# Kernel tuning notes

Hardware: AMD Instinct MI355X
Metric: run time of the kernel (lower is better)

Reference implementation:

```python
import jax, jax.numpy as jnp
import numpy as np

B, N, NF, ND, NH = 16, 128, 64, 100, 64

def glorot(key, shape):
    fan_in, fan_out = shape[0], shape[1]
    limit = np.sqrt(6.0 / (fan_in + fan_out)).astype(np.float32)
    return jax.random.uniform(key, shape, jnp.float32, -limit, limit)

def setup_inputs() -> dict:
    key = jax.random.key(0)
    k1, k2, k3, k4, k5 = jax.random.split(key, 5)
    return {
        "atom_features": jax.random.normal(k1, (B, N, NF), jnp.float32),
        "distance_matrix": jax.random.uniform(k2, (B, N, N, ND), jnp.float32),
        "distance_matrix_mask": jnp.ones((B, N, N), jnp.float32),
        "W_cf": glorot(k3, (NF, NH)),
        "W_df": glorot(k4, (ND, NH)),
        "W_fc": glorot(k5, (NH, NF)),
        "b_cf": jnp.zeros((NH,), jnp.float32),
        "b_df": jnp.zeros((NH,), jnp.float32),
    }

def reference(atom_features, distance_matrix, distance_matrix_mask, W_cf, W_df, W_fc, b_cf, b_df):
    # dist_h: [B, N, N, H]
    dist_h = jnp.einsum('bijd,dh->bijh', distance_matrix, W_df) + b_df
    # atom_h: [B, N, H] -> broadcast over axis 1 (matches tf expand_dims axis=1)
    atom_h = jnp.einsum('bjf,fh->bjh', atom_features, W_cf) + b_cf
    gated = dist_h * atom_h[:, None, :, :]                 # [B, N, N, H]
    out = jnp.einsum('bijh,hf->bijf', gated, W_fc)          # [B, N, N, F]
    out = out * distance_matrix_mask[..., None]
    out = jnp.tanh(out)
    return jnp.sum(out, axis=2) + atom_features             # [B, N, F]
```

## Files before the change

kernel.cpp:

```cpp
#include <hip/hip_runtime.h>
#include <hip/hip_bf16.h>

#define Bsz 16
#define Nn  128
#define NFd 64
#define NDd 100
#define NHd 64

typedef __attribute__((ext_vector_type(8))) short bf16x8;
typedef __attribute__((ext_vector_type(4))) float f32x4;

__device__ __forceinline__ short f2bf(float f) {
  return (short)__builtin_bit_cast(ushort, __float2bfloat16(f));
}

__device__ __forceinline__ float fast_tanh(float x) {
  float e = __expf(2.0f * x);
  return 1.0f - 2.0f * __builtin_amdgcn_rcpf(e + 1.0f);
}

__device__ __forceinline__ void glds16(const float* g, float* l) {
  __builtin_amdgcn_global_load_lds(
      (const __attribute__((address_space(1))) void*)g,
      (__attribute__((address_space(3))) void*)l, 16, 0, 0);
}
__device__ __forceinline__ void glds4(const float* g, float* l) {
  __builtin_amdgcn_global_load_lds(
      (const __attribute__((address_space(1))) void*)g,
      (__attribute__((address_space(3))) void*)l, 4, 0, 0);
}

__global__ __launch_bounds__(256) void prep_kernel(
    const float* __restrict__ AF, const float* __restrict__ Wcf,
    const float* __restrict__ bcf, const float* __restrict__ Wdf,
    const float* __restrict__ Wfc, float* __restrict__ atomh,
    ushort* __restrict__ wdfp, ushort* __restrict__ wfcp,
    float* __restrict__ out) {
  int t = threadIdx.x;
  int blk = blockIdx.x;
  if (blk < 512) {
    int row = blk * 4 + (t >> 6);
    int h = t & 63;
    const float* af = AF + (size_t)row * NFd;
    float a0 = 0.f, a1 = 0.f, a2 = 0.f, a3 = 0.f;
    #pragma unroll 4
    for (int f = 0; f < NFd; f += 4) {
      a0 += af[f + 0] * Wcf[(f + 0) * NHd + h];
      a1 += af[f + 1] * Wcf[(f + 1) * NHd + h];
      a2 += af[f + 2] * Wcf[(f + 2) * NHd + h];
      a3 += af[f + 3] * Wcf[(f + 3) * NHd + h];
    }
    atomh[(size_t)row * NHd + h] = bcf[h] + ((a0 + a1) + (a2 + a3));
  } else if (blk < 544) {
    int idx = (blk - 512) * 256 + t;
    int e = idx & 7;
    int col = (idx >> 3) & 63;
    int grp = idx >> 9;
    int k = grp * 8 + e;
    float v = (k < NDd) ? Wdf[k * NHd + col] : 0.f;
    wdfp[idx] = (ushort)f2bf(v);
  } else if (blk < 560) {
    int idx = (blk - 544) * 256 + t;
    int e = idx & 7;
    int col = (idx >> 3) & 63;
    int grp = idx >> 9;
    int k = grp * 8 + e;
    wfcp[idx] = (ushort)f2bf(Wfc[k * NFd + col]);
  } else {
    int idx = (blk - 560) * 256 + t;
    out[idx] = AF[idx];
  }
}

__global__ __launch_bounds__(256, 6) void dtnn_main_kernel(
    const float* __restrict__ DM,
    const float* __restrict__ MASK,
    const float* __restrict__ bdf,
    const float* __restrict__ atomh,
    const ushort* __restrict__ wdfp,
    const ushort* __restrict__ wfcp,
    float* __restrict__ out) {
  __shared__ float stage[64 * 100];

  const int t    = threadIdx.x;
  const int blk  = blockIdx.x;
  const int bi   = blk >> 1;
  const int half = blk & 1;
  const int b    = bi >> 7;
  const int w    = t >> 6;
  const int lane = t & 63;
  const int p    = t & 15;
  const int q    = (t >> 4) & 3;

  const int jrow = half * 64 + w * 16;

  const float* gsrc = DM + (size_t)bi * (Nn * NDd) + (size_t)jrow * NDd;
  float* lbase = stage + w * 1600;
  #pragma unroll
  for (int v = 0; v < 6; ++v)
    glds16(gsrc + v * 256 + lane * 4, lbase + v * 256);
  glds4(gsrc + 1536 + lane, lbase + 1536);

  asm volatile("s_waitcnt vmcnt(0)" ::: "memory");
  __builtin_amdgcn_sched_barrier(0);

  const bf16x8* wdfv = reinterpret_cast<const bf16x8*>(wdfp);
  const bf16x8* wfcv = reinterpret_cast<const bf16x8*>(wfcp);

  f32x4 acc[4];
  #pragma unroll
  for (int ht = 0; ht < 4; ++ht) {
    float bv = bdf[ht * 16 + p];
    acc[ht] = (f32x4){bv, bv, bv, bv};
  }

  const float* arow = stage + (w * 16 + p) * 100;
  #pragma unroll
  for (int ks = 0; ks < 3; ++ks) {
    float4 x = *reinterpret_cast<const float4*>(arow + ks * 32 + q * 8);
    float4 y = *reinterpret_cast<const float4*>(arow + ks * 32 + q * 8 + 4);
    bf16x8 a;
    a[0] = f2bf(x.x); a[1] = f2bf(x.y); a[2] = f2bf(x.z); a[3] = f2bf(x.w);
    a[4] = f2bf(y.x); a[5] = f2bf(y.y); a[6] = f2bf(y.z); a[7] = f2bf(y.w);
    #pragma unroll
    for (int ht = 0; ht < 4; ++ht)
      acc[ht] = __builtin_amdgcn_mfma_f32_16x16x32_bf16(
          a, wdfv[(ks * 4 + q) * 64 + ht * 16 + p], acc[ht], 0, 0, 0);
  }
  {
    bf16x8 a = (bf16x8){0, 0, 0, 0, 0, 0, 0, 0};
    if (q == 0) {
      float4 x = *reinterpret_cast<const float4*>(arow + 96);
      a[0] = f2bf(x.x); a[1] = f2bf(x.y); a[2] = f2bf(x.z); a[3] = f2bf(x.w);
    }
    #pragma unroll
    for (int ht = 0; ht < 4; ++ht)
      acc[ht] = __builtin_amdgcn_mfma_f32_16x16x32_bf16(
          a, wdfv[(12 + q) * 64 + ht * 16 + p], acc[ht], 0, 0, 0);
  }

  const float* ap = atomh + ((size_t)(b * Nn + jrow + 4 * q)) * NHd + p;
  #pragma unroll
  for (int ht = 0; ht < 4; ++ht) {
    #pragma unroll
    for (int r = 0; r < 4; ++r) acc[ht][r] *= ap[r * NHd + ht * 16];
  }

  ushort* gb = reinterpret_cast<ushort*>(lbase);
  #pragma unroll
  for (int r = 0; r < 4; ++r) {
    int rr = 4 * q + r;
    int sw = (rr & 7) << 3;
    #pragma unroll
    for (int ht = 0; ht < 4; ++ht)
      gb[rr * 64 + ((ht * 16 + p) ^ sw)] = (ushort)f2bf(acc[ht][r]);
  }
  asm volatile("" ::: "memory");

  f32x4 acc2[4];
  #pragma unroll
  for (int ft = 0; ft < 4; ++ft) acc2[ft] = (f32x4){0.f, 0.f, 0.f, 0.f};

  #pragma unroll
  for (int ks = 0; ks < 2; ++ks) {
    int h0 = (ks * 32 + q * 8) ^ ((p & 7) << 3);
    bf16x8 a2 = *reinterpret_cast<const bf16x8*>(&gb[p * 64 + h0]);
    #pragma unroll
    for (int ft = 0; ft < 4; ++ft)
      acc2[ft] = __builtin_amdgcn_mfma_f32_16x16x32_bf16(
          a2, wfcv[(ks * 4 + q) * 64 + ft * 16 + p], acc2[ft], 0, 0, 0);
  }

  float s[4] = {0.f, 0.f, 0.f, 0.f};
  #pragma unroll
  for (int r = 0; r < 4; ++r) {
    float m = MASK[(size_t)bi * Nn + jrow + 4 * q + r];
    #pragma unroll
    for (int ft = 0; ft < 4; ++ft) s[ft] += fast_tanh(acc2[ft][r] * m);
  }

  #pragma unroll
  for (int ft = 0; ft < 4; ++ft) {
    s[ft] += __shfl_xor(s[ft], 16, 64);
    s[ft] += __shfl_xor(s[ft], 32, 64);
  }
  if (q == 0) {
    #pragma unroll
    for (int ft = 0; ft < 4; ++ft)
      unsafeAtomicAdd(&out[(size_t)bi * NFd + ft * 16 + p], s[ft]);
  }
}

extern "C" void kernel_launch(void* const* d_in, const int* in_sizes, int n_in,
                              void* d_out, int out_size, void* d_ws, size_t ws_size,
                              hipStream_t stream) {
  const float* AF   = (const float*)d_in[0];
  const float* DM   = (const float*)d_in[1];
  const float* MASK = (const float*)d_in[2];
  const float* Wcf  = (const float*)d_in[3];
  const float* Wdf  = (const float*)d_in[4];
  const float* Wfc  = (const float*)d_in[5];
  const float* bcf  = (const float*)d_in[6];
  const float* bdf  = (const float*)d_in[7];
  float* out = (float*)d_out;

  float*  atomh = (float*)d_ws;
  ushort* wdfp  = (ushort*)((char*)d_ws + 524288);
  ushort* wfcp  = (ushort*)((char*)d_ws + 524288 + 16384);

  prep_kernel<<<1072, 256, 0, stream>>>(AF, Wcf, bcf, Wdf, Wfc, atomh, wdfp, wfcp, out);
  dtnn_main_kernel<<<2 * Bsz * Nn, 256, 0, stream>>>(DM, MASK, bdf, atomh, wdfp, wfcp, out);
}
```

Baseline: 35.84 us.

## Stage distance tiles in swizzled column chunks and overlap loads with MFMA

Reorganizes the global-to-LDS staging of the distance-matrix tile into three 32-column chunks per row group, stored with an XOR swizzle, plus a separate tail for columns 96-99. The first GEMM then waits on partial vmcnt counts through inline asm, so each chunk's MFMAs can start while later chunks are still loading, rather than waiting for the whole tile. The swizzle is meant to cut LDS bank conflicts on the 128-bit reads. The cost is hand-written waitcnt/ds_read asm that depends on the compiler issuing the loads in a fixed order, which is fragile.

Result: slower. 38.74 us (+8.1%).

```diff
diff --git a/kernel.cpp b/kernel.cpp
--- a/kernel.cpp
+++ b/kernel.cpp
@@ -28,6 +28,20 @@
   __builtin_amdgcn_global_load_lds(
       (const __attribute__((address_space(1))) void*)g,
       (__attribute__((address_space(3))) void*)l, 4, 0, 0);
+}
+
+__device__ __forceinline__ unsigned lds_off(const void* p) {
+  return (unsigned)(uintptr_t)(const __attribute__((address_space(3))) char*)p;
+}
+
+template <int N>
+__device__ __forceinline__ void wait_read2(f32x4& x, f32x4& y, unsigned a0, unsigned a1) {
+  asm volatile("s_waitcnt vmcnt(%4)\n\t"
+               "ds_read_b128 %0, %2\n\t"
+               "ds_read_b128 %1, %3\n\t"
+               "s_waitcnt lgkmcnt(0)"
+               : "=&v"(x), "=&v"(y)
+               : "v"(a0), "v"(a1), "i"(N));
 }
 
 __global__ __launch_bounds__(256) void prep_kernel(
@@ -96,13 +110,19 @@
 
   const float* gsrc = DM + (size_t)bi * (Nn * NDd) + (size_t)jrow * NDd;
   float* lbase = stage + w * 1600;
-  #pragma unroll
-  for (int v = 0; v < 6; ++v)
-    glds16(gsrc + v * 256 + lane * 4, lbase + v * 256);
-  glds4(gsrc + 1536 + lane, lbase + 1536);
-
-  asm volatile("s_waitcnt vmcnt(0)" ::: "memory");
-  __builtin_amdgcn_sched_barrier(0);
+  {
+    const int r8 = lane >> 3, b8 = lane & 7;
+    #pragma unroll
+    for (int c = 0; c < 3; ++c) {
+      #pragma unroll
+      for (int g = 0; g < 2; ++g) {
+        int r = g * 8 + r8;
+        glds16(gsrc + r * 100 + c * 32 + ((b8 ^ (r & 7)) << 2),
+               lbase + c * 512 + g * 256);
+      }
+    }
+    glds4(gsrc + (lane >> 2) * 100 + 96 + (lane & 3), lbase + 1536);
+  }
 
   const bf16x8* wdfv = reinterpret_cast<const bf16x8*>(wdfp);
   const bf16x8* wfcv = reinterpret_cast<const bf16x8*>(wfcp);
@@ -114,24 +134,35 @@
     acc[ht] = (f32x4){bv, bv, bv, bv};
   }
 
-  const float* arow = stage + (w * 16 + p) * 100;
-  #pragma unroll
-  for (int ks = 0; ks < 3; ++ks) {
-    float4 x = *reinterpret_cast<const float4*>(arow + ks * 32 + q * 8);
-    float4 y = *reinterpret_cast<const float4*>(arow + ks * 32 + q * 8 + 4);
-    bf16x8 a;
-    a[0] = f2bf(x.x); a[1] = f2bf(x.y); a[2] = f2bf(x.z); a[3] = f2bf(x.w);
-    a[4] = f2bf(y.x); a[5] = f2bf(y.y); a[6] = f2bf(y.z); a[7] = f2bf(y.w);
-    #pragma unroll
-    for (int ht = 0; ht < 4; ++ht)
-      acc[ht] = __builtin_amdgcn_mfma_f32_16x16x32_bf16(
-          a, wdfv[(ks * 4 + q) * 64 + ht * 16 + p], acc[ht], 0, 0, 0);
-  }
+  const unsigned sbase = lds_off(lbase);
+  const unsigned arow  = sbase + p * 128;
+  const unsigned bsw0  = ((2 * q) ^ (p & 7)) << 4;
+  f32x4 x, y;
+
+  #define P1_CHUNK(KS, NW)                                                     \
+  {                                                                            \
+    unsigned a0 = arow + KS * 2048 + bsw0;                                     \
+    wait_read2<NW>(x, y, a0, a0 ^ 16);                                         \
+    bf16x8 a;                                                                  \
+    a[0] = f2bf(x[0]); a[1] = f2bf(x[1]); a[2] = f2bf(x[2]); a[3] = f2bf(x[3]);\
+    a[4] = f2bf(y[0]); a[5] = f2bf(y[1]); a[6] = f2bf(y[2]); a[7] = f2bf(y[3]);\
+    _Pragma("unroll")                                                          \
+    for (int ht = 0; ht < 4; ++ht)                                             \
+      acc[ht] = __builtin_amdgcn_mfma_f32_16x16x32_bf16(                       \
+          a, wdfv[(KS * 4 + q) * 64 + ht * 16 + p], acc[ht], 0, 0, 0);         \
+  }
+  P1_CHUNK(0, 5)
+  P1_CHUNK(1, 3)
+  P1_CHUNK(2, 1)
+  #undef P1_CHUNK
+
   {
+    asm volatile("s_waitcnt vmcnt(0)" ::: "memory");
+    __builtin_amdgcn_sched_barrier(0);
     bf16x8 a = (bf16x8){0, 0, 0, 0, 0, 0, 0, 0};
     if (q == 0) {
-      float4 x = *reinterpret_cast<const float4*>(arow + 96);
-      a[0] = f2bf(x.x); a[1] = f2bf(x.y); a[2] = f2bf(x.z); a[3] = f2bf(x.w);
+      float4 tx = *reinterpret_cast<const float4*>(lbase + 1536 + p * 4);
+      a[0] = f2bf(tx.x); a[1] = f2bf(tx.y); a[2] = f2bf(tx.z); a[3] = f2bf(tx.w);
     }
     #pragma unroll
     for (int ht = 0; ht < 4; ++ht)
```

## Swizzle DM LDS staging, transpose atom_h, prefetch gate/mask before wait

Applied to the files above, without the earlier changes.

Distance-matrix tiles are now staged into LDS in 32-column chunks with an XOR swizzle, so the MFMA A-fragment reads avoid bank conflicts. atom_h is stored transposed so each lane reads its four gating values with one vector load, and those loads plus the mask and bias loads are issued before the single vmcnt wait, overlapping with the DM transfer. The copy of atom_features into the output is folded into the atom_h prep blocks, which drops 512 prep blocks. Occupancy hint for the main kernel drops from 6 to 4 waves, which may lower latency hiding in exchange for more registers.

Result: slower. 41.65 us (+16.2%).

```diff
diff --git a/kernel.cpp b/kernel.cpp
--- a/kernel.cpp
+++ b/kernel.cpp
@@ -33,7 +33,7 @@
 __global__ __launch_bounds__(256) void prep_kernel(
     const float* __restrict__ AF, const float* __restrict__ Wcf,
     const float* __restrict__ bcf, const float* __restrict__ Wdf,
-    const float* __restrict__ Wfc, float* __restrict__ atomh,
+    const float* __restrict__ Wfc, float* __restrict__ atomhT,
     ushort* __restrict__ wdfp, ushort* __restrict__ wfcp,
     float* __restrict__ out) {
   int t = threadIdx.x;
@@ -50,7 +50,9 @@
       a2 += af[f + 2] * Wcf[(f + 2) * NHd + h];
       a3 += af[f + 3] * Wcf[(f + 3) * NHd + h];
     }
-    atomh[(size_t)row * NHd + h] = bcf[h] + ((a0 + a1) + (a2 + a3));
+    int b = row >> 7, j = row & 127;
+    atomhT[((size_t)(b * NHd + h)) << 7 | j] = bcf[h] + ((a0 + a1) + (a2 + a3));
+    out[(size_t)row * NFd + h] = af[h];
   } else if (blk < 544) {
     int idx = (blk - 512) * 256 + t;
     int e = idx & 7;
@@ -59,28 +61,25 @@
     int k = grp * 8 + e;
     float v = (k < NDd) ? Wdf[k * NHd + col] : 0.f;
     wdfp[idx] = (ushort)f2bf(v);
-  } else if (blk < 560) {
+  } else {
     int idx = (blk - 544) * 256 + t;
     int e = idx & 7;
     int col = (idx >> 3) & 63;
     int grp = idx >> 9;
     int k = grp * 8 + e;
     wfcp[idx] = (ushort)f2bf(Wfc[k * NFd + col]);
-  } else {
-    int idx = (blk - 560) * 256 + t;
-    out[idx] = AF[idx];
-  }
-}
-
-__global__ __launch_bounds__(256, 6) void dtnn_main_kernel(
+  }
+}
+
+__global__ __launch_bounds__(256, 4) void dtnn_main_kernel(
     const float* __restrict__ DM,
     const float* __restrict__ MASK,
     const float* __restrict__ bdf,
-    const float* __restrict__ atomh,
+    const float* __restrict__ atomhT,
     const ushort* __restrict__ wdfp,
     const ushort* __restrict__ wfcp,
     float* __restrict__ out) {
-  __shared__ float stage[64 * 100];
+  __shared__ float stage[4 * 1600];
 
   const int t    = threadIdx.x;
   const int blk  = blockIdx.x;
@@ -95,33 +94,49 @@
   const int jrow = half * 64 + w * 16;
 
   const float* gsrc = DM + (size_t)bi * (Nn * NDd) + (size_t)jrow * NDd;
-  float* lbase = stage + w * 1600;
-  #pragma unroll
-  for (int v = 0; v < 6; ++v)
-    glds16(gsrc + v * 256 + lane * 4, lbase + v * 256);
-  glds4(gsrc + 1536 + lane, lbase + 1536);
+  float* lb = stage + w * 1600;
+  {
+    const int r8 = lane >> 3, b8 = lane & 7;
+    #pragma unroll
+    for (int c = 0; c < 3; ++c) {
+      #pragma unroll
+      for (int g = 0; g < 2; ++g) {
+        int r = g * 8 + r8;
+        glds16(gsrc + r * 100 + c * 32 + ((b8 ^ (r & 7)) << 2),
+               lb + c * 512 + g * 256);
+      }
+    }
+    glds4(gsrc + (lane >> 2) * 100 + 96 + (lane & 3), lb + 1536);
+  }
+
+  const bf16x8* wdfv = reinterpret_cast<const bf16x8*>(wdfp);
+  const bf16x8* wfcv = reinterpret_cast<const bf16x8*>(wfcp);
+
+  f32x4 ah[4];
+  #pragma unroll
+  for (int ht = 0; ht < 4; ++ht)
+    ah[ht] = *reinterpret_cast<const f32x4*>(
+        atomhT + (((size_t)(b * NHd + ht * 16 + p)) << 7) + jrow + 4 * q);
+  f32x4 mv = *reinterpret_cast<const f32x4*>(MASK + (size_t)bi * Nn + jrow + 4 * q);
+  float bv[4];
+  #pragma unroll
+  for (int ht = 0; ht < 4; ++ht) bv[ht] = bdf[ht * 16 + p];
 
   asm volatile("s_waitcnt vmcnt(0)" ::: "memory");
   __builtin_amdgcn_sched_barrier(0);
 
-  const bf16x8* wdfv = reinterpret_cast<const bf16x8*>(wdfp);
-  const bf16x8* wfcv = reinterpret_cast<const bf16x8*>(wfcp);
-
   f32x4 acc[4];
   #pragma unroll
-  for (int ht = 0; ht < 4; ++ht) {
-    float bv = bdf[ht * 16 + p];
-    acc[ht] = (f32x4){bv, bv, bv, bv};
-  }
-
-  const float* arow = stage + (w * 16 + p) * 100;
+  for (int ht = 0; ht < 4; ++ht) acc[ht] = (f32x4){bv[ht], bv[ht], bv[ht], bv[ht]};
+
   #pragma unroll
   for (int ks = 0; ks < 3; ++ks) {
-    float4 x = *reinterpret_cast<const float4*>(arow + ks * 32 + q * 8);
-    float4 y = *reinterpret_cast<const float4*>(arow + ks * 32 + q * 8 + 4);
+    const float* cbase = lb + ks * 512 + p * 32;
+    f32x4 x = *reinterpret_cast<const f32x4*>(cbase + (((2 * q)     ) ^ (p & 7)) * 4);
+    f32x4 y = *reinterpret_cast<const f32x4*>(cbase + (((2 * q) + 1 ) ^ (p & 7)) * 4);
     bf16x8 a;
-    a[0] = f2bf(x.x); a[1] = f2bf(x.y); a[2] = f2bf(x.z); a[3] = f2bf(x.w);
-    a[4] = f2bf(y.x); a[5] = f2bf(y.y); a[6] = f2bf(y.z); a[7] = f2bf(y.w);
+    a[0] = f2bf(x[0]); a[1] = f2bf(x[1]); a[2] = f2bf(x[2]); a[3] = f2bf(x[3]);
+    a[4] = f2bf(y[0]); a[5] = f2bf(y[1]); a[6] = f2bf(y[2]); a[7] = f2bf(y[3]);
     #pragma unroll
     for (int ht = 0; ht < 4; ++ht)
       acc[ht] = __builtin_amdgcn_mfma_f32_16x16x32_bf16(
@@ -130,8 +145,8 @@
   {
     bf16x8 a = (bf16x8){0, 0, 0, 0, 0, 0, 0, 0};
     if (q == 0) {
-      float4 x = *reinterpret_cast<const float4*>(arow + 96);
-      a[0] = f2bf(x.x); a[1] = f2bf(x.y); a[2] = f2bf(x.z); a[3] = f2bf(x.w);
+      f32x4 tx = *reinterpret_cast<const f32x4*>(lb + 1536 + 4 * p);
+      a[0] = f2bf(tx[0]); a[1] = f2bf(tx[1]); a[2] = f2bf(tx[2]); a[3] = f2bf(tx[3]);
     }
     #pragma unroll
     for (int ht = 0; ht < 4; ++ht)
@@ -139,14 +154,13 @@
           a, wdfv[(12 + q) * 64 + ht * 16 + p], acc[ht], 0, 0, 0);
   }
 
-  const float* ap = atomh + ((size_t)(b * Nn + jrow + 4 * q)) * NHd + p;
   #pragma unroll
   for (int ht = 0; ht < 4; ++ht) {
     #pragma unroll
-    for (int r = 0; r < 4; ++r) acc[ht][r] *= ap[r * NHd + ht * 16];
-  }
-
-  ushort* gb = reinterpret_cast<ushort*>(lbase);
+    for (int r = 0; r < 4; ++r) acc[ht][r] *= ah[ht][r];
+  }
+
+  ushort* gb = reinterpret_cast<ushort*>(lb);
   #pragma unroll
   for (int r = 0; r < 4; ++r) {
     int rr = 4 * q + r;
@@ -174,9 +188,8 @@
   float s[4] = {0.f, 0.f, 0.f, 0.f};
   #pragma unroll
   for (int r = 0; r < 4; ++r) {
-    float m = MASK[(size_t)bi * Nn + jrow + 4 * q + r];
-    #pragma unroll
-    for (int ft = 0; ft < 4; ++ft) s[ft] += fast_tanh(acc2[ft][r] * m);
+    #pragma unroll
+    for (int ft = 0; ft < 4; ++ft) s[ft] += fast_tanh(acc2[ft][r] * mv[r]);
   }
 
   #pragma unroll
@@ -204,10 +217,10 @@
   const float* bdf  = (const float*)d_in[7];
   float* out = (float*)d_out;
 
-  float*  atomh = (float*)d_ws;
-  ushort* wdfp  = (ushort*)((char*)d_ws + 524288);
-  ushort* wfcp  = (ushort*)((char*)d_ws + 524288 + 16384);
-
-  prep_kernel<<<1072, 256, 0, stream>>>(AF, Wcf, bcf, Wdf, Wfc, atomh, wdfp, wfcp, out);
-  dtnn_main_kernel<<<2 * Bsz * Nn, 256, 0, stream>>>(DM, MASK, bdf, atomh, wdfp, wfcp, out);
-}
+  float*  atomhT = (float*)d_ws;
+  ushort* wdfp   = (ushort*)((char*)d_ws + 524288);
+  ushort* wfcp   = (ushort*)((char*)d_ws + 524288 + 16384);
+
+  prep_kernel<<<560, 256, 0, stream>>>(AF, Wcf, bcf, Wdf, Wfc, atomhT, wdfp, wfcp, out);
+  dtnn_main_kernel<<<2 * Bsz * Nn, 256, 0, stream>>>(DM, MASK, bdf, atomhT, wdfp, wfcp, out);
+}
```
